# Performance work log

Measured on AMD Instinct MI355X. Metric: run time of the kernel, lower is better.

## Reference

```python
import jax, jax.numpy as jnp
import numpy as np

B, M, A = 64, 16, 128
H = 128            # cfg.SUB.DIM
P = 16             # NUM_PHYSICOCHEMICAL
NUM_ATOM_TYPES = 100
NUM_FP_TYPES = 2048
EPS_W = 1e-8
EPS_LN = 1e-5


def setup_inputs() -> dict:
    key = jax.random.key(0)
    ks = jax.random.split(key, 16)
    def xavier(k, shape):
        fan_in, fan_out = shape[0], shape[-1]
        lim = float(np.sqrt(6.0 / (fan_in + fan_out)))
        return jax.random.uniform(k, shape, jnp.float32, -lim, lim)
    return {
        "atom_features": jax.random.randint(ks[0], (B, M, A), 0, NUM_ATOM_TYPES),
        "fingerprints": jax.random.randint(ks[1], (B, M, A), 0, NUM_FP_TYPES),
        "phys": jax.random.normal(ks[2], (B, M, P), jnp.float32),
        "ratios": jax.random.uniform(ks[3], (B, M), jnp.float32),
        # learned params
        "atom_emb": xavier(ks[4], (NUM_ATOM_TYPES, H)),
        "fp_emb": xavier(ks[5], (NUM_FP_TYPES, H)),
        "W_in": xavier(ks[6], (2 * H, H)),
        "b_in": jnp.zeros((H,), jnp.float32),
        "ln_g": jnp.ones((H + P,), jnp.float32),
        "ln_b": jnp.zeros((H + P,), jnp.float32),
        "W1": xavier(ks[7], (H + P, H)),
        "b1": jnp.zeros((H,), jnp.float32),
        "W2": xavier(ks[8], (H, 1)),
        "b2": jnp.zeros((1,), jnp.float32),
    }


def reference(atom_features, fingerprints, phys, ratios,
              atom_emb, fp_emb, W_in, b_in, ln_g, ln_b, W1, b1, W2, b2):
    # per-molecule embed: gather both tables, concat, linear, relu, mean over atoms
    e = jnp.concatenate([atom_emb[atom_features], fp_emb[fingerprints]], axis=-1)  # [B,M,A,2H]
    h = jax.nn.relu(jnp.einsum('bmad,dh->bmah', e, W_in) + b_in)                   # [B,M,A,H]
    mol = h.mean(axis=2)                                                           # [B,M,H]

    pv = jnp.nan_to_num(phys, nan=0.0, posinf=1000.0, neginf=-1000.0)              # [B,M,P]

    # normalized mixing weights per batch item
    w = ratios / (ratios.sum(axis=1, keepdims=True) + EPS_W)                       # [B,M]
    mix_h = jnp.einsum('bm,bmh->bh', w, mol)                                       # [B,H]
    mix_p = jnp.einsum('bm,bmp->bp', w, pv)                                        # [B,P]

    z = jnp.concatenate([mix_h, mix_p], axis=-1)                                   # [B,H+P]
    # head: LayerNorm -> Linear -> ReLU -> Linear (dropout p=0, eval)
    mu = z.mean(axis=-1, keepdims=True)
    var = ((z - mu) ** 2).mean(axis=-1, keepdims=True)
    zn = (z - mu) / jnp.sqrt(var + EPS_LN) * ln_g + ln_b
    y = jax.nn.relu(zn @ W1 + b1) @ W2 + b2                                        # [B,1]
    return jnp.nan_to_num(y)
```

## Files before the change

### kernel.cpp

```cpp
#include <hip/hip_runtime.h>
#include <math.h>
#include <float.h>

#define B_ 64
#define M_ 16
#define A_ 128
#define H_ 128
#define P_ 16
#define NAT 100
#define NFP 2048
#define ZDIM (H_ + P_)

__device__ float g_Ta[NAT * H_];
__device__ float g_Tf[NFP * H_];
__device__ float g_mol[B_ * M_ * H_];

__global__ void k1_precompute(const float* __restrict__ atom_emb,
                              const float* __restrict__ fp_emb,
                              const float* __restrict__ W_in) {
    __shared__ float e[H_];
    const int r = blockIdx.x, j = threadIdx.x;
    const float* emb;
    const float* W;
    float* out;
    if (r < NAT) { emb = atom_emb + r * H_; W = W_in;             out = g_Ta + r * H_; }
    else { int rf = r - NAT; emb = fp_emb + rf * H_; W = W_in + H_ * H_; out = g_Tf + rf * H_; }
    e[j] = emb[j];
    __syncthreads();
    float acc = 0.f;
#pragma unroll 8
    for (int k = 0; k < H_; ++k) acc += e[k] * W[k * H_ + j];
    out[j] = acc;
}

__global__ void k2_mol(const int* __restrict__ af, const int* __restrict__ fpi,
                       const float* __restrict__ b_in) {
    __shared__ int ia[A_];
    __shared__ int ifp[A_];
    const int bm = blockIdx.x, j = threadIdx.x;
    ia[j]  = af[bm * A_ + j];
    ifp[j] = fpi[bm * A_ + j];
    __syncthreads();
    const float bj = b_in[j];
    float acc = 0.f;
#pragma unroll 8
    for (int a = 0; a < A_; ++a) {
        float v = g_Ta[ia[a] * H_ + j] + g_Tf[ifp[a] * H_ + j] + bj;
        acc += fmaxf(v, 0.f);
    }
    g_mol[bm * H_ + j] = acc * (1.0f / (float)A_);
}

__global__ void k3_head(const float* __restrict__ phys,
                        const float* __restrict__ ratios,
                        const float* __restrict__ ln_g,
                        const float* __restrict__ ln_b,
                        const float* __restrict__ W1,
                        const float* __restrict__ b1,
                        const float* __restrict__ W2,
                        const float* __restrict__ b2,
                        float* __restrict__ out) {
    const int b = blockIdx.x, j = threadIdx.x;
    __shared__ float w[M_];
    __shared__ float z[ZDIM];
    __shared__ float zn[ZDIM];
    __shared__ float red[H_];

    if (j < M_) w[j] = ratios[b * M_ + j];
    __syncthreads();

    float rsum = 0.f;
#pragma unroll
    for (int m = 0; m < M_; ++m) rsum += w[m];
    const float dinv = 1.0f / (rsum + 1e-8f);

    float acc = 0.f;
#pragma unroll
    for (int m = 0; m < M_; ++m) acc += (w[m] * dinv) * g_mol[(b * M_ + m) * H_ + j];
    z[j] = acc;

    if (j < P_) {
        float accp = 0.f;
#pragma unroll
        for (int m = 0; m < M_; ++m) {
            float pv = phys[(b * M_ + m) * P_ + j];
            if (isnan(pv)) pv = 0.f;
            else if (isinf(pv)) pv = (pv > 0.f) ? 1000.f : -1000.f;
            accp += (w[m] * dinv) * pv;
        }
        z[H_ + j] = accp;
    }
    __syncthreads();

    float s = 0.f;
#pragma unroll 8
    for (int k = 0; k < ZDIM; ++k) s += z[k];
    const float mu = s * (1.0f / (float)ZDIM);
    float s2 = 0.f;
#pragma unroll 8
    for (int k = 0; k < ZDIM; ++k) { float d = z[k] - mu; s2 += d * d; }
    const float rstd = rsqrtf(s2 * (1.0f / (float)ZDIM) + 1e-5f);

    for (int k = j; k < ZDIM; k += H_)
        zn[k] = (z[k] - mu) * rstd * ln_g[k] + ln_b[k];
    __syncthreads();

    float a1 = 0.f;
#pragma unroll 8
    for (int k = 0; k < ZDIM; ++k) a1 += zn[k] * W1[k * H_ + j];
    const float h1 = fmaxf(a1 + b1[j], 0.f);
    red[j] = h1 * W2[j];
    __syncthreads();

    if (j == 0) {
        float y = b2[0];
#pragma unroll 8
        for (int k = 0; k < H_; ++k) y += red[k];
        if (isnan(y)) y = 0.f;
        else if (isinf(y)) y = (y > 0.f) ? FLT_MAX : -FLT_MAX;
        out[b] = y;
    }
}

extern "C" void kernel_launch(void* const* d_in, const int* in_sizes, int n_in,
                              void* d_out, int out_size, void* d_ws, size_t ws_size,
                              hipStream_t stream) {
    const int*   af    = (const int*)d_in[0];
    const int*   fpi   = (const int*)d_in[1];
    const float* phys  = (const float*)d_in[2];
    const float* ratio = (const float*)d_in[3];
    const float* aemb  = (const float*)d_in[4];
    const float* femb  = (const float*)d_in[5];
    const float* W_in  = (const float*)d_in[6];
    const float* b_in  = (const float*)d_in[7];
    const float* ln_g  = (const float*)d_in[8];
    const float* ln_b  = (const float*)d_in[9];
    const float* W1    = (const float*)d_in[10];
    const float* b1    = (const float*)d_in[11];
    const float* W2    = (const float*)d_in[12];
    const float* b2    = (const float*)d_in[13];
    float* out = (float*)d_out;

    k1_precompute<<<dim3(NAT + NFP), dim3(H_), 0, stream>>>(aemb, femb, W_in);
    k2_mol<<<dim3(B_ * M_), dim3(H_), 0, stream>>>(af, fpi, b_in);
    k3_head<<<dim3(B_), dim3(H_), 0, stream>>>(phys, ratio, ln_g, ln_b, W1, b1, W2, b2, out);
}
```

Before: 108.5 us.

## Fuse three kernels into one cooperative persistent kernel with grid syncs

Replaces the three separate launches (table precompute, per-molecule gather-mean, head) with a single cooperative kernel of 512 blocks of 256 threads. Each block handles two rows at a time, and the phases are separated by grid.sync(). This removes two kernel launch boundaries and their gaps. The cost is grid-wide barrier overhead and fewer resident blocks than the original per-row launch, so each block loops over several rows.

```diff
diff --git a/kernel.cpp b/kernel.cpp
--- a/kernel.cpp
+++ b/kernel.cpp
@@ -1,6 +1,9 @@
 #include <hip/hip_runtime.h>
+#include <hip/hip_cooperative_groups.h>
 #include <math.h>
 #include <float.h>
+
+namespace cg = cooperative_groups;
 
 #define B_ 64
 #define M_ 16
@@ -10,115 +13,128 @@
 #define NAT 100
 #define NFP 2048
 #define ZDIM (H_ + P_)
+#define NROWS (NAT + NFP)
+#define NBM (B_ * M_)
+#define GRID 512
 
 __device__ float g_Ta[NAT * H_];
 __device__ float g_Tf[NFP * H_];
-__device__ float g_mol[B_ * M_ * H_];
+__device__ float g_mol[NBM * H_];
 
-__global__ void k1_precompute(const float* __restrict__ atom_emb,
-                              const float* __restrict__ fp_emb,
-                              const float* __restrict__ W_in) {
-    __shared__ float e[H_];
-    const int r = blockIdx.x, j = threadIdx.x;
-    const float* emb;
-    const float* W;
-    float* out;
-    if (r < NAT) { emb = atom_emb + r * H_; W = W_in;             out = g_Ta + r * H_; }
-    else { int rf = r - NAT; emb = fp_emb + rf * H_; W = W_in + H_ * H_; out = g_Tf + rf * H_; }
-    e[j] = emb[j];
-    __syncthreads();
-    float acc = 0.f;
+__global__ __launch_bounds__(256, 4)
+void fused_kernel(const int* __restrict__ af, const int* __restrict__ fpi,
+                  const float* __restrict__ phys, const float* __restrict__ ratios,
+                  const float* __restrict__ aemb, const float* __restrict__ femb,
+                  const float* __restrict__ W_in, const float* __restrict__ b_in,
+                  const float* __restrict__ ln_g, const float* __restrict__ ln_b,
+                  const float* __restrict__ W1, const float* __restrict__ b1,
+                  const float* __restrict__ W2, const float* __restrict__ b2,
+                  float* __restrict__ out) {
+    cg::grid_group grid = cg::this_grid();
+    const int t = threadIdx.x;
+    const int j = t & (H_ - 1);
+    const int half = t >> 7;
+    const int g = blockIdx.x;
+
+    __shared__ float e_sh[2][H_];
+    __shared__ int ia[2][A_];
+    __shared__ int ifp[2][A_];
+
+    for (int r = g * 2 + half; r < NROWS; r += gridDim.x * 2) {
+        const float* emb; const float* W; float* o;
+        if (r < NAT) { emb = aemb + r * H_; W = W_in;            o = g_Ta + r * H_; }
+        else { int rf = r - NAT; emb = femb + rf * H_; W = W_in + H_ * H_; o = g_Tf + rf * H_; }
+        e_sh[half][j] = emb[j];
+        __syncthreads();
+        float acc = 0.f;
 #pragma unroll 8
-    for (int k = 0; k < H_; ++k) acc += e[k] * W[k * H_ + j];
-    out[j] = acc;
-}
+        for (int k = 0; k < H_; ++k) acc += e_sh[half][k] * W[k * H_ + j];
+        o[j] = acc;
+        __syncthreads();
+    }
 
-__global__ void k2_mol(const int* __restrict__ af, const int* __restrict__ fpi,
-                       const float* __restrict__ b_in) {
-    __shared__ int ia[A_];
-    __shared__ int ifp[A_];
-    const int bm = blockIdx.x, j = threadIdx.x;
-    ia[j]  = af[bm * A_ + j];
-    ifp[j] = fpi[bm * A_ + j];
-    __syncthreads();
-    const float bj = b_in[j];
-    float acc = 0.f;
+    grid.sync();
+
+    for (int bm = g * 2 + half; bm < NBM; bm += gridDim.x * 2) {
+        ia[half][j]  = af[bm * A_ + j];
+        ifp[half][j] = fpi[bm * A_ + j];
+        __syncthreads();
+        const float bj = b_in[j];
+        float acc = 0.f;
 #pragma unroll 8
-    for (int a = 0; a < A_; ++a) {
-        float v = g_Ta[ia[a] * H_ + j] + g_Tf[ifp[a] * H_ + j] + bj;
-        acc += fmaxf(v, 0.f);
+        for (int a = 0; a < A_; ++a) {
+            float v = g_Ta[ia[half][a] * H_ + j] + g_Tf[ifp[half][a] * H_ + j] + bj;
+            acc += fmaxf(v, 0.f);
+        }
+        g_mol[bm * H_ + j] = acc * (1.0f / (float)A_);
+        __syncthreads();
     }
-    g_mol[bm * H_ + j] = acc * (1.0f / (float)A_);
-}
 
-__global__ void k3_head(const float* __restrict__ phys,
-                        const float* __restrict__ ratios,
-                        const float* __restrict__ ln_g,
-                        const float* __restrict__ ln_b,
-                        const float* __restrict__ W1,
-                        const float* __restrict__ b1,
-                        const float* __restrict__ W2,
-                        const float* __restrict__ b2,
-                        float* __restrict__ out) {
-    const int b = blockIdx.x, j = threadIdx.x;
-    __shared__ float w[M_];
-    __shared__ float z[ZDIM];
-    __shared__ float zn[ZDIM];
-    __shared__ float red[H_];
+    grid.sync();
 
-    if (j < M_) w[j] = ratios[b * M_ + j];
-    __syncthreads();
+    if (g < B_) {
+        __shared__ float w[M_];
+        __shared__ float z[ZDIM];
+        __shared__ float zn[ZDIM];
+        __shared__ float red[H_];
+        const int b = g;
 
-    float rsum = 0.f;
+        if (t < M_) w[t] = ratios[b * M_ + t];
+        __syncthreads();
+
+        float rsum = 0.f;
 #pragma unroll
-    for (int m = 0; m < M_; ++m) rsum += w[m];
-    const float dinv = 1.0f / (rsum + 1e-8f);
+        for (int m = 0; m < M_; ++m) rsum += w[m];
+        const float dinv = 1.0f / (rsum + 1e-8f);
 
-    float acc = 0.f;
+        if (t < H_) {
+            float acc = 0.f;
 #pragma unroll
-    for (int m = 0; m < M_; ++m) acc += (w[m] * dinv) * g_mol[(b * M_ + m) * H_ + j];
-    z[j] = acc;
+            for (int m = 0; m < M_; ++m) acc += (w[m] * dinv) * g_mol[(b * M_ + m) * H_ + t];
+            z[t] = acc;
+        } else if (t < H_ + P_) {
+            const int p = t - H_;
+            float accp = 0.f;
+#pragma unroll
+            for (int m = 0; m < M_; ++m) {
+                float pv = phys[(b * M_ + m) * P_ + p];
+                if (isnan(pv)) pv = 0.f;
+                else if (isinf(pv)) pv = (pv > 0.f) ? 1000.f : -1000.f;
+                accp += (w[m] * dinv) * pv;
+            }
+            z[H_ + p] = accp;
+        }
+        __syncthreads();
 
-    if (j < P_) {
-        float accp = 0.f;
-#pragma unroll
-        for (int m = 0; m < M_; ++m) {
-            float pv = phys[(b * M_ + m) * P_ + j];
-            if (isnan(pv)) pv = 0.f;
-            else if (isinf(pv)) pv = (pv > 0.f) ? 1000.f : -1000.f;
-            accp += (w[m] * dinv) * pv;
+        float s = 0.f;
+#pragma unroll 8
+        for (int k = 0; k < ZDIM; ++k) s += z[k];
+        const float mu = s * (1.0f / (float)ZDIM);
+        float s2 = 0.f;
+#pragma unroll 8
+        for (int k = 0; k < ZDIM; ++k) { float d = z[k] - mu; s2 += d * d; }
+        const float rstd = rsqrtf(s2 * (1.0f / (float)ZDIM) + 1e-5f);
+
+        if (t < ZDIM) zn[t] = (z[t] - mu) * rstd * ln_g[t] + ln_b[t];
+        __syncthreads();
+
+        if (t < H_) {
+            float a1 = 0.f;
+#pragma unroll 8
+            for (int k = 0; k < ZDIM; ++k) a1 += zn[k] * W1[k * H_ + t];
+            const float h1 = fmaxf(a1 + b1[t], 0.f);
+            red[t] = h1 * W2[t];
         }
-        z[H_ + j] = accp;
-    }
-    __syncthreads();
+        __syncthreads();
 
-    float s = 0.f;
+        if (t == 0) {
+            float y = b2[0];
 #pragma unroll 8
-    for (int k = 0; k < ZDIM; ++k) s += z[k];
-    const float mu = s * (1.0f / (float)ZDIM);
-    float s2 = 0.f;
-#pragma unroll 8
-    for (int k = 0; k < ZDIM; ++k) { float d = z[k] - mu; s2 += d * d; }
-    const float rstd = rsqrtf(s2 * (1.0f / (float)ZDIM) + 1e-5f);
-
-    for (int k = j; k < ZDIM; k += H_)
-        zn[k] = (z[k] - mu) * rstd * ln_g[k] + ln_b[k];
-    __syncthreads();
-
-    float a1 = 0.f;
-#pragma unroll 8
-    for (int k = 0; k < ZDIM; ++k) a1 += zn[k] * W1[k * H_ + j];
-    const float h1 = fmaxf(a1 + b1[j], 0.f);
-    red[j] = h1 * W2[j];
-    __syncthreads();
-
-    if (j == 0) {
-        float y = b2[0];
-#pragma unroll 8
-        for (int k = 0; k < H_; ++k) y += red[k];
-        if (isnan(y)) y = 0.f;
-        else if (isinf(y)) y = (y > 0.f) ? FLT_MAX : -FLT_MAX;
-        out[b] = y;
+            for (int k = 0; k < H_; ++k) y += red[k];
+            if (isnan(y)) y = 0.f;
+            else if (isinf(y)) y = (y > 0.f) ? FLT_MAX : -FLT_MAX;
+            out[b] = y;
+        }
     }
 }
 
@@ -141,7 +157,12 @@
     const float* b2    = (const float*)d_in[13];
     float* out = (float*)d_out;
 
-    k1_precompute<<<dim3(NAT + NFP), dim3(H_), 0, stream>>>(aemb, femb, W_in);
-    k2_mol<<<dim3(B_ * M_), dim3(H_), 0, stream>>>(af, fpi, b_in);
-    k3_head<<<dim3(B_), dim3(H_), 0, stream>>>(phys, ratio, ln_g, ln_b, W1, b1, W2, b2, out);
+    void* args[] = {
+        (void*)&af, (void*)&fpi, (void*)&phys, (void*)&ratio,
+        (void*)&aemb, (void*)&femb, (void*)&W_in, (void*)&b_in,
+        (void*)&ln_g, (void*)&ln_b, (void*)&W1, (void*)&b1,
+        (void*)&W2, (void*)&b2, (void*)&out
+    };
+    hipLaunchCooperativeKernel((const void*)fused_kernel,
+                               dim3(GRID), dim3(256), args, 0, stream);
 }
```

Result: slower. 250.9 us (+131.1%).
